# Kernel tuning notes

Hardware: AMD Instinct MI355X
Metric: run time of the kernel (lower is better)

## Reference

```python
import jax, jax.numpy as jnp
import numpy as np

D = 48


def setup_inputs() -> dict:
    key = jax.random.key(0)
    k1, k2, k3, k4, k5 = jax.random.split(key, 5)
    B, N, d = 4, 512, D
    x = jax.random.normal(k1, (B, N, d), dtype=jnp.float32)
    # Linear(2d, 2d) and Linear(2d, d); stored as (in, out) so y = x @ W + b
    s1 = 1.0 / np.sqrt(2 * d)
    W1 = jax.random.uniform(k2, (2 * d, 2 * d), dtype=jnp.float32, minval=-s1, maxval=s1)
    b1 = jax.random.uniform(k3, (2 * d,), dtype=jnp.float32, minval=-s1, maxval=s1)
    W2 = jax.random.uniform(k4, (2 * d, d), dtype=jnp.float32, minval=-s1, maxval=s1)
    b2 = jax.random.uniform(k5, (d,), dtype=jnp.float32, minval=-s1, maxval=s1)
    return {"x": x, "W1": W1, "b1": b1, "W2": W2, "b2": b2}


def reference(x, W1, b1, W2, b2):
    B, N, d = x.shape
    # pairwise concat: [B, N, N, 2d] with (i, j) = (x_i, x_j)
    xi = jnp.broadcast_to(x[:, :, None, :], (B, N, N, d))
    xj = jnp.broadcast_to(x[:, None, :, :], (B, N, N, d))
    cat = jnp.concatenate([xi, xj], axis=-1)
    h = jax.nn.gelu(cat @ W1 + b1, approximate=False)  # torch GELU is exact erf form
    p = h @ W2 + b2  # [B, N, N, d]
    mask = jnp.triu(jnp.ones((N, N), dtype=bool), 1)  # j > i masked
    p = jnp.where(mask[None, :, :, None], 0.0, p)
    w = jnp.sqrt(jnp.sum(p * p, axis=-1))  # frobenius norm over feature dim -> [B, N, N]
    w = jnp.where(mask[None, :, :], -1e9, w)
    w = jax.nn.softmax(w, axis=-1)[..., None]  # softmax over j
    return jnp.sum(w * p, axis=2)  # [B, N, d]
```

## Files before the change

kernel.cpp:

```cpp
#include <hip/hip_runtime.h>
#include <hip/hip_bf16.h>
#include <hip/hip_fp16.h>
#include <math.h>

#define DD 48
#define NN 512
#define TWO_D 96
#define ROWS 2048

typedef __attribute__((ext_vector_type(8))) _Float16 f16x8;
typedef __attribute__((ext_vector_type(4))) float f32x4;
typedef __attribute__((ext_vector_type(2))) float f32x2;
typedef __attribute__((ext_vector_type(4))) unsigned int u32x4;

__device__ __forceinline__ __half2 h2cast(unsigned int u) { return __builtin_bit_cast(__half2, u); }

__device__ __forceinline__ f32x2 gelu_poly2(f32x2 u) {
    f32x2 lim;  lim  = 3.5777f;
    f32x2 nlim; nlim = -3.5777f;
    const f32x2 uc = __builtin_elementwise_min(__builtin_elementwise_max(u, nlim), lim);
    const f32x2 v = uc * uc;
    f32x2 c5; c5 = -1.04448e-6f;
    f32x2 c4; c4 = 4.61896e-5f;
    f32x2 c3; c3 = -8.62284e-4f;
    f32x2 c2; c2 = 9.22138e-3f;
    f32x2 c1; c1 = -6.58353e-2f;
    f32x2 c0; c0 = 3.98855e-1f;
    f32x2 E = __builtin_elementwise_fma(v, c5, c4);
    E = __builtin_elementwise_fma(v, E, c3);
    E = __builtin_elementwise_fma(v, E, c2);
    E = __builtin_elementwise_fma(v, E, c1);
    E = __builtin_elementwise_fma(v, E, c0);
    f32x2 hlf; hlf = 0.5f;
    return u * __builtin_elementwise_fma(uc, E, hlf);
}

__global__ __launch_bounds__(256) void precompute_kernel(
        const float* __restrict__ x,
        const float* __restrict__ W1,
        const float* __restrict__ b1,
        const float* __restrict__ W2,
        __half* __restrict__ Aout,
        __half* __restrict__ Bout,
        __half* __restrict__ W2T) {
    if (blockIdx.x == ROWS / 4) {
        for (int idx = threadIdx.x; idx < DD * TWO_D; idx += 256) {
            const int f = idx / TWO_D;
            const int k = idx - f * TWO_D;
            W2T[idx] = __float2half(W2[k * DD + f]);
        }
        return;
    }
    const int wave = threadIdx.x >> 6;
    const int lane = threadIdx.x & 63;
    const int row = blockIdx.x * 4 + wave;
    __shared__ float xs[4][DD];
    if (threadIdx.x < 4 * DD)
        xs[threadIdx.x / DD][threadIdx.x % DD] = x[blockIdx.x * 4 * DD + threadIdx.x];
    __syncthreads();
    for (int t = lane; t < TWO_D; t += 64) {
        float a0 = 0.f, a1 = 0.f;
#pragma unroll 8
        for (int k = 0; k < DD; ++k) {
            const float xv = xs[wave][k];
            a0 = fmaf(xv, W1[k * TWO_D + t], a0);
            a1 = fmaf(xv, W1[(DD + k) * TWO_D + t], a1);
        }
        Aout[row * TWO_D + t] = __float2half(a0 + b1[t]);
        Bout[row * TWO_D + t] = __float2half(a1);
    }
}

#define STREAM_KS(PB_, ACC_, PF_, NPTR_, KS_)                                   \
  { const u32x4 aw = avp[KS_];                                                  \
    const u32x4 bw = PB_[KS_];                                                  \
    if (PF_) PB_[KS_] = *(const u32x4*)&(NPTR_)[(KS_) * 32 + q8];               \
    const __half2 u0 = __hadd2(h2cast(aw.x), h2cast(bw.x));                     \
    const __half2 u1 = __hadd2(h2cast(aw.y), h2cast(bw.y));                     \
    const __half2 u2 = __hadd2(h2cast(aw.z), h2cast(bw.z));                     \
    const __half2 u3 = __hadd2(h2cast(aw.w), h2cast(bw.w));                     \
    f32x2 f0, f1, f2, f3;                                                       \
    { float2 t_ = __half22float2(u0); f0.x = t_.x; f0.y = t_.y; }               \
    { float2 t_ = __half22float2(u1); f1.x = t_.x; f1.y = t_.y; }               \
    { float2 t_ = __half22float2(u2); f2.x = t_.x; f2.y = t_.y; }               \
    { float2 t_ = __half22float2(u3); f3.x = t_.x; f3.y = t_.y; }               \
    const f32x2 g0 = gelu_poly2(f0);                                            \
    const f32x2 g1 = gelu_poly2(f1);                                            \
    const f32x2 g2 = gelu_poly2(f2);                                            \
    const f32x2 g3 = gelu_poly2(f3);                                            \
    union { f16x8 v; __half2 h2[4]; } hf;                                       \
    hf.h2[0] = __float22half2_rn(make_float2(g0.x, g0.y));                      \
    hf.h2[1] = __float22half2_rn(make_float2(g1.x, g1.y));                      \
    hf.h2[2] = __float22half2_rn(make_float2(g2.x, g2.y));                      \
    hf.h2[3] = __float22half2_rn(make_float2(g3.x, g3.y));                      \
    ACC_[0] = __builtin_amdgcn_mfma_f32_16x16x32_f16(bfrag[0][KS_], hf.v, ACC_[0], 0, 0, 0); \
    ACC_[1] = __builtin_amdgcn_mfma_f32_16x16x32_f16(bfrag[1][KS_], hf.v, ACC_[1], 0, 0, 0); \
    ACC_[2] = __builtin_amdgcn_mfma_f32_16x16x32_f16(bfrag[2][KS_], hf.v, ACC_[2], 0, 0, 0); \
  }

#define CHUNK_EPI(J0_, I_, ACC_, L_, O_)                                        \
  { f32x2 pv[3][2];                                                             \
    f32x2 ss2; ss2 = 0.f;                                                       \
    _Pragma("unroll")                                                           \
    for (int t = 0; t < 3; ++t) {                                               \
      pv[t][0].x = ACC_[t][0]; pv[t][0].y = ACC_[t][1];                         \
      pv[t][1].x = ACC_[t][2]; pv[t][1].y = ACC_[t][3];                         \
      ss2 = __builtin_elementwise_fma(pv[t][0], pv[t][0], ss2);                 \
      ss2 = __builtin_elementwise_fma(pv[t][1], pv[t][1], ss2);                 \
    }                                                                           \
    float ss = ss2.x + ss2.y;                                                   \
    ss += __shfl_xor(ss, 16);                                                   \
    ss += __shfl_xor(ss, 32);                                                   \
    const int j = (J0_) + n;                                                    \
    const float ew = (j <= (I_))                                                \
        ? __builtin_amdgcn_exp2f(sqrtf(ss) * 1.44269504f) : 0.f;                \
    L_ += ew;                                                                   \
    f32x2 ew2; ew2 = ew;                                                        \
    _Pragma("unroll")                                                           \
    for (int t = 0; t < 3; ++t) {                                               \
      O_[t][0] = __builtin_elementwise_fma(ew2, pv[t][0], O_[t][0]);            \
      O_[t][1] = __builtin_elementwise_fma(ew2, pv[t][1], O_[t][1]);            \
    } }

#define PROCESS_ROW_DUAL(I_, ROW_, CSTART_, L_, O_)                             \
  { u32x4 avp[3];                                                               \
    _Pragma("unroll")                                                           \
    for (int ks = 0; ks < 3; ++ks)                                              \
      avp[ks] = *(const u32x4*)&Arow[(size_t)(ROW_) * TWO_D + ks * 32 + q8];    \
    const int nch = ((I_) + 16) >> 4;                                           \
    int c = (CSTART_);                                                          \
    const __half* __restrict__ Bp = Bbase + (size_t)((c << 4) + n) * TWO_D;     \
    u32x4 pbA[3], pbB[3];                                                       \
    if (c < nch) {                                                              \
      _Pragma("unroll")                                                         \
      for (int ks = 0; ks < 3; ++ks) pbA[ks] = *(const u32x4*)&Bp[ks * 32 + q8];\
    }                                                                           \
    if (c + 4 < nch) {                                                          \
      const __half* __restrict__ B2_ = Bp + 64 * TWO_D;                         \
      _Pragma("unroll")                                                         \
      for (int ks = 0; ks < 3; ++ks) pbB[ks] = *(const u32x4*)&B2_[ks * 32 + q8];\
    }                                                                           \
    for (; c + 4 < nch; c += 8) {                                               \
      const bool pfA = (c + 8) < nch;                                           \
      const bool pfB = (c + 12) < nch;                                          \
      const __half* __restrict__ BpA = Bp + 128 * TWO_D;                        \
      const __half* __restrict__ BpB = Bp + 192 * TWO_D;                        \
      f32x4 accA[3], accB[3];                                                   \
      accA[0] = b2q[0]; accA[1] = b2q[1]; accA[2] = b2q[2];                     \
      accB[0] = b2q[0]; accB[1] = b2q[1]; accB[2] = b2q[2];                     \
      _Pragma("unroll")                                                         \
      for (int ksi = 0; ksi < 3; ++ksi) {                                       \
        STREAM_KS(pbA, accA, pfA, BpA, ksi);                                    \
        STREAM_KS(pbB, accB, pfB, BpB, ksi);                                    \
      }                                                                         \
      CHUNK_EPI((c << 4), I_, accA, L_, O_);                                    \
      CHUNK_EPI(((c + 4) << 4), I_, accB, L_, O_);                              \
      Bp = BpA;                                                                 \
    }                                                                           \
    if (c < nch) {                                                              \
      f32x4 accA[3];                                                            \
      accA[0] = b2q[0]; accA[1] = b2q[1]; accA[2] = b2q[2];                     \
      _Pragma("unroll")                                                         \
      for (int ksi = 0; ksi < 3; ++ksi) { STREAM_KS(pbA, accA, false, Bp, ksi); } \
      CHUNK_EPI((c << 4), I_, accA, L_, O_);                                    \
    } }

#define REDUCE_FLUSH(L_, O_, SEL_)                                              \
  { _Pragma("unroll")                                                           \
    for (int d = 1; d <= 8; d <<= 1) {                                          \
      L_ += __shfl_xor(L_, d);                                                  \
      _Pragma("unroll")                                                         \
      for (int t = 0; t < 3; ++t)                                               \
        _Pragma("unroll")                                                       \
        for (int r = 0; r < 2; ++r) {                                           \
          O_[t][r].x += __shfl_xor(O_[t][r].x, d);                              \
          O_[t][r].y += __shfl_xor(O_[t][r].y, d);                              \
        }                                                                       \
    }                                                                           \
    if (n == 0) {                                                               \
      _Pragma("unroll")                                                         \
      for (int t = 0; t < 3; ++t)                                               \
        _Pragma("unroll")                                                       \
        for (int r = 0; r < 2; ++r) {                                           \
          ored[wave][SEL_][t * 16 + 4 * q + 2 * r + 0] = O_[t][r].x;            \
          ored[wave][SEL_][t * 16 + 4 * q + 2 * r + 1] = O_[t][r].y;            \
        }                                                                       \
      if (q == 0) lred[wave][SEL_] = L_;                                        \
    } }

__global__ __launch_bounds__(256) void pair_softmax_kernel(
        const __half* __restrict__ Arow,
        const __half* __restrict__ Brow,
        const __half* __restrict__ W2T,
        const float* __restrict__ b2,
        float* __restrict__ out) {
    const int batch = blockIdx.x >> 8;
    const int pr = blockIdx.x & 255;
    const int iH = (NN - 1) - pr;
    const int iL = pr;
    const int cH = (iH >> 4) + 1;
    const int rowH = batch * NN + iH;
    const int rowL = batch * NN + iL;
    const __half* __restrict__ Bbase = Brow + (size_t)batch * NN * TWO_D;

    const int tid = threadIdx.x;
    const int wave = tid >> 6;
    const int lane = tid & 63;
    const int n = lane & 15;
    const int q = lane >> 4;
    const int q8 = q * 8;

    __shared__ float lred[4][2];
    __shared__ float ored[4][2][DD];

    f16x8 bfrag[3][3];
#pragma unroll
    for (int t = 0; t < 3; ++t)
#pragma unroll
        for (int ks = 0; ks < 3; ++ks)
            bfrag[t][ks] = *(const f16x8*)&W2T[(t * 16 + n) * TWO_D + ks * 32 + q8];
    f32x4 b2q[3];
#pragma unroll
    for (int t = 0; t < 3; ++t)
        b2q[t] = *(const f32x4*)&b2[t * 16 + 4 * q];

    const int cstartL = (wave + 128 - cH) & 3;

    float lH = 0.f;
    f32x2 oH[3][2];
#pragma unroll
    for (int t = 0; t < 3; ++t)
#pragma unroll
        for (int r = 0; r < 2; ++r) oH[t][r] = 0.f;
    PROCESS_ROW_DUAL(iH, rowH, wave, lH, oH);
    REDUCE_FLUSH(lH, oH, 0);

    float lL = 0.f;
    f32x2 oL[3][2];
#pragma unroll
    for (int t = 0; t < 3; ++t)
#pragma unroll
        for (int r = 0; r < 2; ++r) oL[t][r] = 0.f;
    PROCESS_ROW_DUAL(iL, rowL, cstartL, lL, oL);
    REDUCE_FLUSH(lL, oL, 1);

    __syncthreads();
    if (tid < 2 * DD) {
        const int sel = tid / DD;
        const int f = tid - sel * DD;
        float L = 0.f, O = 0.f;
#pragma unroll
        for (int wv = 0; wv < 4; ++wv) {
            L += lred[wv][sel];
            O += ored[wv][sel][f];
        }
        const int row = sel ? rowL : rowH;
        out[row * DD + f] = O / L;
    }
}

extern "C" void kernel_launch(void* const* d_in, const int* in_sizes, int n_in,
                              void* d_out, int out_size, void* d_ws, size_t ws_size,
                              hipStream_t stream) {
    const float* x  = (const float*)d_in[0];
    const float* W1 = (const float*)d_in[1];
    const float* b1 = (const float*)d_in[2];
    const float* W2 = (const float*)d_in[3];
    const float* b2 = (const float*)d_in[4];
    float* outp = (float*)d_out;

    __half* A   = (__half*)d_ws;
    __half* Bb  = A + ROWS * TWO_D;
    __half* W2T = Bb + ROWS * TWO_D;

    precompute_kernel<<<ROWS / 4 + 1, 256, 0, stream>>>(x, W1, b1, W2, A, Bb, W2T);
    pair_softmax_kernel<<<1024, 256, 0, stream>>>(A, Bb, W2T, b2, outp);
}
```

Before: 91.27 us.

## Software-pipeline chunk epilogue one iteration behind MFMA stream

New measurement: 89.69 us. About the same (-1.7%).

```diff
diff --git a/kernel.cpp b/kernel.cpp
--- a/kernel.cpp
+++ b/kernel.cpp
@@ -71,10 +71,10 @@
     }
 }
 
-#define STREAM_KS(PB_, ACC_, PF_, NPTR_, KS_)                                   \
+#define STREAM_KS(PB_, ACC_, NPTR_, KS_)                                        \
   { const u32x4 aw = avp[KS_];                                                  \
     const u32x4 bw = PB_[KS_];                                                  \
-    if (PF_) PB_[KS_] = *(const u32x4*)&(NPTR_)[(KS_) * 32 + q8];               \
+    PB_[KS_] = *(const u32x4*)&(NPTR_)[(KS_) * 32 + q8];                        \
     const __half2 u0 = __hadd2(h2cast(aw.x), h2cast(bw.x));                     \
     const __half2 u1 = __hadd2(h2cast(aw.y), h2cast(bw.y));                     \
     const __half2 u2 = __hadd2(h2cast(aw.z), h2cast(bw.z));                     \
@@ -98,71 +98,68 @@
     ACC_[2] = __builtin_amdgcn_mfma_f32_16x16x32_f16(bfrag[2][KS_], hf.v, ACC_[2], 0, 0, 0); \
   }
 
-#define CHUNK_EPI(J0_, I_, ACC_, L_, O_)                                        \
-  { f32x2 pv[3][2];                                                             \
-    f32x2 ss2; ss2 = 0.f;                                                       \
-    _Pragma("unroll")                                                           \
-    for (int t = 0; t < 3; ++t) {                                               \
-      pv[t][0].x = ACC_[t][0]; pv[t][0].y = ACC_[t][1];                         \
-      pv[t][1].x = ACC_[t][2]; pv[t][1].y = ACC_[t][3];                         \
-      ss2 = __builtin_elementwise_fma(pv[t][0], pv[t][0], ss2);                 \
-      ss2 = __builtin_elementwise_fma(pv[t][1], pv[t][1], ss2);                 \
-    }                                                                           \
-    float ss = ss2.x + ss2.y;                                                   \
-    ss += __shfl_xor(ss, 16);                                                   \
-    ss += __shfl_xor(ss, 32);                                                   \
-    const int j = (J0_) + n;                                                    \
-    const float ew = (j <= (I_))                                                \
-        ? __builtin_amdgcn_exp2f(sqrtf(ss) * 1.44269504f) : 0.f;                \
+#define EPI_CONSUME(L_, O_)                                                     \
+  { const float full = (ssp + s1p) + (s2p + s3p);                               \
+    const float ew = ((jp + n) <= rowi)                                         \
+        ? __builtin_amdgcn_exp2f(sqrtf(full) * 1.44269504f) : 0.f;              \
     L_ += ew;                                                                   \
     f32x2 ew2; ew2 = ew;                                                        \
     _Pragma("unroll")                                                           \
     for (int t = 0; t < 3; ++t) {                                               \
-      O_[t][0] = __builtin_elementwise_fma(ew2, pv[t][0], O_[t][0]);            \
-      O_[t][1] = __builtin_elementwise_fma(ew2, pv[t][1], O_[t][1]);            \
+      O_[t][0] = __builtin_elementwise_fma(ew2, pvp[t][0], O_[t][0]);           \
+      O_[t][1] = __builtin_elementwise_fma(ew2, pvp[t][1], O_[t][1]);           \
     } }
 
-#define PROCESS_ROW_DUAL(I_, ROW_, CSTART_, L_, O_)                             \
-  { u32x4 avp[3];                                                               \
+#define PROCESS_ROW_PIPE(I_, ROW_, CSTART_, L_, O_)                             \
+  { const int rowi = (I_);                                                      \
+    u32x4 avp[3];                                                               \
     _Pragma("unroll")                                                           \
     for (int ks = 0; ks < 3; ++ks)                                              \
       avp[ks] = *(const u32x4*)&Arow[(size_t)(ROW_) * TWO_D + ks * 32 + q8];    \
-    const int nch = ((I_) + 16) >> 4;                                           \
+    const int nch = (rowi + 16) >> 4;                                           \
     int c = (CSTART_);                                                          \
-    const __half* __restrict__ Bp = Bbase + (size_t)((c << 4) + n) * TWO_D;     \
-    u32x4 pbA[3], pbB[3];                                                       \
     if (c < nch) {                                                              \
-      _Pragma("unroll")                                                         \
-      for (int ks = 0; ks < 3; ++ks) pbA[ks] = *(const u32x4*)&Bp[ks * 32 + q8];\
-    }                                                                           \
-    if (c + 4 < nch) {                                                          \
-      const __half* __restrict__ B2_ = Bp + 64 * TWO_D;                         \
-      _Pragma("unroll")                                                         \
-      for (int ks = 0; ks < 3; ++ks) pbB[ks] = *(const u32x4*)&B2_[ks * 32 + q8];\
-    }                                                                           \
-    for (; c + 4 < nch; c += 8) {                                               \
-      const bool pfA = (c + 8) < nch;                                           \
-      const bool pfB = (c + 12) < nch;                                          \
-      const __half* __restrict__ BpA = Bp + 128 * TWO_D;                        \
-      const __half* __restrict__ BpB = Bp + 192 * TWO_D;                        \
-      f32x4 accA[3], accB[3];                                                   \
-      accA[0] = b2q[0]; accA[1] = b2q[1]; accA[2] = b2q[2];                     \
-      accB[0] = b2q[0]; accB[1] = b2q[1]; accB[2] = b2q[2];                     \
-      _Pragma("unroll")                                                         \
-      for (int ksi = 0; ksi < 3; ++ksi) {                                       \
-        STREAM_KS(pbA, accA, pfA, BpA, ksi);                                    \
-        STREAM_KS(pbB, accB, pfB, BpB, ksi);                                    \
+      const __half* __restrict__ Bp = Bbase + (size_t)((c << 4) + n) * TWO_D;   \
+      u32x4 pb[3];                                                              \
+      _Pragma("unroll")                                                         \
+      for (int ks = 0; ks < 3; ++ks) pb[ks] = *(const u32x4*)&Bp[ks * 32 + q8]; \
+      f32x2 pvp[3][2];                                                          \
+      _Pragma("unroll")                                                         \
+      for (int t = 0; t < 3; ++t) { pvp[t][0] = 0.f; pvp[t][1] = 0.f; }         \
+      float ssp = 0.f, s1p = 0.f, s2p = 0.f, s3p = 0.f;                         \
+      int jp = 0x40000000;                         \
+      for (; c < nch; c += 4) {                                                 \
+        const __half* __restrict__ Bn =                                         \
+            ((c + 4) < nch) ? Bp + 64 * TWO_D : Bp;       \
+        f32x4 acc[3];                                                           \
+        acc[0] = b2q[0]; acc[1] = b2q[1]; acc[2] = b2q[2];                      \
+        _Pragma("unroll")                                                       \
+        for (int ksi = 0; ksi < 3; ++ksi) { STREAM_KS(pb, acc, Bn, ksi); }      \
+                         \
+        f32x2 ss2; ss2 = 0.f;                                                   \
+        _Pragma("unroll")                                                       \
+        for (int t = 0; t < 3; ++t) {                                           \
+          f32x2 p01; p01.x = acc[t][0]; p01.y = acc[t][1];                      \
+          f32x2 p23; p23.x = acc[t][2]; p23.y = acc[t][3];                      \
+          ss2 = __builtin_elementwise_fma(p01, p01, ss2);                       \
+          ss2 = __builtin_elementwise_fma(p23, p23, ss2);                       \
+        }                                                                       \
+        const float ss = ss2.x + ss2.y;                                         \
+        const float s1 = __shfl_xor(ss, 16);                                    \
+        const float s2 = __shfl_xor(ss, 32);                                    \
+        const float s3 = __shfl_xor(ss, 48);                                    \
+                \
+        EPI_CONSUME(L_, O_);                                                    \
+                                                              \
+        _Pragma("unroll")                                                       \
+        for (int t = 0; t < 3; ++t) {                                           \
+          pvp[t][0].x = acc[t][0]; pvp[t][0].y = acc[t][1];                     \
+          pvp[t][1].x = acc[t][2]; pvp[t][1].y = acc[t][3];                     \
+        }                                                                       \
+        ssp = ss; s1p = s1; s2p = s2; s3p = s3; jp = c << 4;                    \
+        Bp = Bn;                                                                \
       }                                                                         \
-      CHUNK_EPI((c << 4), I_, accA, L_, O_);                                    \
-      CHUNK_EPI(((c + 4) << 4), I_, accB, L_, O_);                              \
-      Bp = BpA;                                                                 \
-    }                                                                           \
-    if (c < nch) {                                                              \
-      f32x4 accA[3];                                                            \
-      accA[0] = b2q[0]; accA[1] = b2q[1]; accA[2] = b2q[2];                     \
-      _Pragma("unroll")                                                         \
-      for (int ksi = 0; ksi < 3; ++ksi) { STREAM_KS(pbA, accA, false, Bp, ksi); } \
-      CHUNK_EPI((c << 4), I_, accA, L_, O_);                                    \
+      EPI_CONSUME(L_, O_);                    \
     } }
 
 #define REDUCE_FLUSH(L_, O_, SEL_)                                              \
@@ -232,7 +229,7 @@
     for (int t = 0; t < 3; ++t)
 #pragma unroll
         for (int r = 0; r < 2; ++r) oH[t][r] = 0.f;
-    PROCESS_ROW_DUAL(iH, rowH, wave, lH, oH);
+    PROCESS_ROW_PIPE(iH, rowH, wave, lH, oH);
     REDUCE_FLUSH(lH, oH, 0);
 
     float lL = 0.f;
@@ -241,7 +238,7 @@
     for (int t = 0; t < 3; ++t)
 #pragma unroll
         for (int r = 0; r < 2; ++r) oL[t][r] = 0.f;
-    PROCESS_ROW_DUAL(iL, rowL, cstartL, lL, oL);
+    PROCESS_ROW_PIPE(iL, rowL, cstartL, lL, oL);
     REDUCE_FLUSH(lL, oL, 1);
 
     __syncthreads();
```
